# Kernel tuning notes

Hardware: AMD Instinct MI355X
Metric: run time of the kernel (lower is better)

Reference implementation:

```python
import jax, jax.numpy as jnp
import numpy as np

HEADS = 16
DIM_HEAD = 64
SCALE = DIM_HEAD ** -0.5
EPS = 1e-5


def layer_norm(x, gamma):
    mu = jnp.mean(x, axis=-1, keepdims=True)
    var = jnp.var(x, axis=-1, keepdims=True)
    return (x - mu) * jax.lax.rsqrt(var + EPS) * gamma


def setup_inputs() -> dict:
    key = jax.random.key(0)
    ks = jax.random.split(key, 5)
    B, S, D = 2, 2048, 1024
    x = jax.random.normal(ks[0], (B, S, D), dtype=jnp.float32)
    gamma = jnp.ones((D,), dtype=jnp.float32)
    Wq = jax.random.normal(ks[1], (D, HEADS * DIM_HEAD), dtype=jnp.float32) * (D ** -0.5)
    Wkv = jax.random.normal(ks[2], (D, 2 * DIM_HEAD), dtype=jnp.float32) * (D ** -0.5)
    Wo = jax.random.normal(ks[3], (HEADS * DIM_HEAD, D), dtype=jnp.float32) * ((HEADS * DIM_HEAD) ** -0.5)
    return {"x": x, "gamma": gamma, "Wq": Wq, "Wkv": Wkv, "Wo": Wo}


def reference(x, gamma, Wq, Wkv, Wo):
    B, S, D = x.shape
    kv_input = x  # context=None -> self attention
    xn = layer_norm(x, gamma)
    q = xn @ Wq                          # [B,S,H*Dh]
    kv = kv_input @ Wkv                  # [B,S,2*Dh]
    k, v = jnp.split(kv, 2, axis=-1)     # each [B,S,Dh]
    q = q.reshape(B, S, HEADS, DIM_HEAD).transpose(0, 2, 1, 3) * SCALE  # [B,H,S,Dh]
    sim = jnp.einsum('bhid,bjd->bhij', q, k)  # [B,H,S,S]
    # causal mask: triu(j - i + 1) masked
    i_idx = jnp.arange(S)[:, None]
    j_idx = jnp.arange(S)[None, :]
    neg = -jnp.finfo(sim.dtype).max
    sim = jnp.where(j_idx > i_idx, neg, sim)
    attn = jax.nn.softmax(sim, axis=-1)
    out = jnp.einsum('bhij,bjd->bhid', attn, v)  # [B,H,S,Dh]
    out = out.transpose(0, 2, 1, 3).reshape(B, S, HEADS * DIM_HEAD)
    return out @ Wo
```

## Files before the change

### kernel.cpp

```cpp
#include <hip/hip_runtime.h>

typedef unsigned short u16;
typedef __attribute__((ext_vector_type(8))) u16    u16x8;
typedef __attribute__((ext_vector_type(4))) u16    u16x4;
typedef __attribute__((ext_vector_type(2))) unsigned u32x2;
typedef __attribute__((ext_vector_type(8))) __bf16 bf16x8;
typedef __attribute__((ext_vector_type(4))) float  f32x4;
typedef __attribute__((ext_vector_type(16))) float f32x16;

__device__ __forceinline__ u16 f2bf(float f) {
    unsigned u = __float_as_uint(f);
    u += 0x7fffu + ((u >> 16) & 1u);
    return (u16)(u >> 16);
}
__device__ __forceinline__ bf16x8 ldbf8(const u16* p) {
    return __builtin_bit_cast(bf16x8, *(const u16x8*)p);
}
__device__ __forceinline__ f32x4 mfma16(bf16x8 a, bf16x8 b, f32x4 c) {
    return __builtin_amdgcn_mfma_f32_16x16x32_bf16(a, b, c, 0, 0, 0);
}
__device__ __forceinline__ f32x16 mfma32x(bf16x8 a, bf16x8 b, f32x16 c) {
    return __builtin_amdgcn_mfma_f32_32x32x16_bf16(a, b, c, 0, 0, 0);
}
__device__ __forceinline__ float exp2a(float x) {
    float r; asm("v_exp_f32 %0, %1" : "=v"(r) : "v"(x)); return r;
}
__device__ __forceinline__ unsigned cvtpk(float lo, float hiv) {
    unsigned r; asm("v_cvt_pk_bf16_f32 %0, %1, %2" : "=v"(r) : "v"(lo), "v"(hiv)); return r;
}
__device__ __forceinline__ u32x2 permswap2(unsigned a, unsigned b) {
    return __builtin_amdgcn_permlane32_swap(a, b, false, false);
}
__device__ __forceinline__ float combine_sum(float x) {
    u32x2 pr = permswap2(__float_as_uint(x), __float_as_uint(x));
    return __uint_as_float(pr[0]) + __uint_as_float(pr[1]);
}
__device__ __forceinline__ bf16x8 pack4(unsigned a, unsigned b, unsigned c, unsigned d) {
    union { unsigned u[4]; bf16x8 v; } t; t.u[0] = a; t.u[1] = b; t.u[2] = c; t.u[3] = d; return t.v;
}

__global__ void transpose_cast_all(const float* __restrict__ Wq, const float* __restrict__ Wkv,
                                   const float* __restrict__ Wo, u16* __restrict__ Wq_t,
                                   u16* __restrict__ Wkv_t, u16* __restrict__ Wo_t, float qscale) {
    __shared__ float tile[32][33];
    int by = blockIdx.y;
    const float* W; u16* Wt; int N; float scale;
    if (by < 32)      { W = Wq;  Wt = Wq_t;  N = 1024; scale = qscale; }
    else if (by < 36) { W = Wkv; Wt = Wkv_t; N = 128;  by -= 32; scale = 1.0f; }
    else              { W = Wo;  Wt = Wo_t;  N = 1024; by -= 36; scale = 1.0f; }
    const int K = 1024;
    int kb = blockIdx.x * 32, nb = by * 32;
    int tx = threadIdx.x, ty = threadIdx.y;
#pragma unroll
    for (int i = 0; i < 32; i += 8)
        tile[ty + i][tx] = W[(size_t)(kb + ty + i) * N + nb + tx];
    __syncthreads();
#pragma unroll
    for (int i = 0; i < 32; i += 8)
        Wt[(size_t)(nb + ty + i) * K + kb + tx] = f2bf(tile[tx][ty + i] * scale);
}

__global__ __launch_bounds__(256) void ln_cast(const float* __restrict__ x, const float* __restrict__ gamma,
                                               u16* __restrict__ xn, u16* __restrict__ xb) {
    const int row = blockIdx.x;
    const int t = threadIdx.x;
    const float4 v = ((const float4*)(x + (size_t)row * 1024))[t];
    float s  = v.x + v.y + v.z + v.w;
    float s2 = v.x * v.x + v.y * v.y + v.z * v.z + v.w * v.w;
#pragma unroll
    for (int off = 32; off; off >>= 1) { s += __shfl_down(s, off); s2 += __shfl_down(s2, off); }
    __shared__ float red[2][4];
    const int w = t >> 6, lane = t & 63;
    if (lane == 0) { red[0][w] = s; red[1][w] = s2; }
    __syncthreads();
    s  = red[0][0] + red[0][1] + red[0][2] + red[0][3];
    s2 = red[1][0] + red[1][1] + red[1][2] + red[1][3];
    const float mu  = s * (1.0f / 1024.0f);
    const float var = s2 * (1.0f / 1024.0f) - mu * mu;
    const float rs  = rsqrtf(var + 1e-5f);
    const float4 g = ((const float4*)gamma)[t];
    u16x4 on, ob;
    on.x = f2bf((v.x - mu) * rs * g.x); on.y = f2bf((v.y - mu) * rs * g.y);
    on.z = f2bf((v.z - mu) * rs * g.z); on.w = f2bf((v.w - mu) * rs * g.w);
    ob.x = f2bf(v.x); ob.y = f2bf(v.y); ob.z = f2bf(v.z); ob.w = f2bf(v.w);
    ((u16x4*)(xn + (size_t)row * 1024))[t] = on;
    ((u16x4*)(xb + (size_t)row * 1024))[t] = ob;
}

template<int BM, int BN, int BK, int EPI>
__global__ __launch_bounds__(256, 2) void gemm_bt(const u16* __restrict__ A, const u16* __restrict__ Bt,
                                                  u16* __restrict__ Cb, float* __restrict__ Cf,
                                                  u16* __restrict__ Cv, int M, int N, int K) {
    constexpr int WM = BM / 2, WN = BN / 2, FM = WM / 16, FN = WN / 16;
    constexpr int CPR = BK / 8;
    constexpr int MS = CPR - 1;
    constexpr int CHA = BM * CPR, CH = (BM + BN) * CPR, ITERS = CH / 256;
    __shared__ __align__(16) u16 lds[2][(BM + BN) * BK];
    __shared__ float kred[2][64];
    const int tid = threadIdx.x;
    const int nwg = gridDim.x * gridDim.y;
    int lin = blockIdx.x + gridDim.x * blockIdx.y;
    lin = (lin & 7) * (nwg >> 3) + (lin >> 3);
    const int bx = lin % gridDim.x, by = lin / gridDim.x;
    const int m0 = bx * BM, n0 = by * BN;
    const int w = tid >> 6, lane = tid & 63, cl = lane & 15, kg = lane >> 4;
    const int wr = w >> 1, wc = w & 1;

    auto stage = [&](int buf, int k0) {
#pragma unroll
        for (int it = 0; it < ITERS; ++it) {
            int c = it * 256 + tid;
            const u16* g;
            if (c < CHA) { int r = c / CPR, cc = c & MS; g = A  + (size_t)(m0 + r) * K + k0 + ((cc ^ (r & MS)) * 8); }
            else { int c2 = c - CHA; int r = c2 / CPR, cc = c2 & MS; g = Bt + (size_t)(n0 + r) * K + k0 + ((cc ^ (r & MS)) * 8); }
            __builtin_amdgcn_global_load_lds(
                (const __attribute__((address_space(1))) unsigned int*)g,
                (__attribute__((address_space(3))) unsigned int*)&lds[buf][c * 8], 16, 0, 0);
        }
    };

    const f32x4 zero = {0.f, 0.f, 0.f, 0.f};
    f32x4 acc[FM][FN];
#pragma unroll
    for (int m = 0; m < FM; m++)
#pragma unroll
        for (int n = 0; n < FN; n++) acc[m][n] = zero;

    const int KT = K / BK;
    stage(0, 0);
    for (int t = 0; t < KT; ++t) {
        __syncthreads();
        if (t + 1 < KT) stage((t + 1) & 1, (t + 1) * BK);
        const u16* As = &lds[t & 1][0];
        const u16* Bs = &lds[t & 1][BM * BK];
#pragma unroll
        for (int s = 0; s < BK / 32; s++) {
            bf16x8 af[FM], bfr[FN];
#pragma unroll
            for (int m = 0; m < FM; m++) {
                const int ra = wr * WM + m * 16 + cl;
                af[m] = ldbf8(As + ra * BK + (((s * 4 + kg) ^ (ra & MS)) * 8));
            }
#pragma unroll
            for (int n = 0; n < FN; n++) {
                const int rb = wc * WN + n * 16 + cl;
                bfr[n] = ldbf8(Bs + rb * BK + (((s * 4 + kg) ^ (rb & MS)) * 8));
            }
#pragma unroll
            for (int m = 0; m < FM; m++)
#pragma unroll
                for (int n = 0; n < FN; n++) acc[m][n] = mfma16(af[m], bfr[n], acc[m][n]);
        }
    }

#pragma unroll
    for (int m = 0; m < FM; m++)
#pragma unroll
        for (int n = 0; n < FN; n++)
#pragma unroll
            for (int r = 0; r < 4; r++) {
                const int row = m0 + wr * WM + m * 16 + kg * 4 + r;
                const int col = n0 + wc * WN + n * 16 + cl;
                const float v = acc[m][n][r];
                if constexpr (EPI == 0) Cb[(size_t)row * N + col] = f2bf(v);
                else if constexpr (EPI == 1) Cf[(size_t)row * N + col] = v;
                else {
                    if (col < 64) Cb[(size_t)row * 64 + col] = f2bf(v);
                    else { int bb = row >> 11, s = row & 2047;
                           Cv[((size_t)bb * 64 + (col - 64)) * 2048 + s] = f2bf(v); }
                }
            }

    if constexpr (EPI == 2) {
        if (n0 == 0) {
            float s2[FM][4];
#pragma unroll
            for (int m = 0; m < FM; m++)
#pragma unroll
                for (int r = 0; r < 4; r++) {
                    float t = 0.f;
#pragma unroll
                    for (int n = 0; n < FN; n++) {
                        const float vb = __uint_as_float(((unsigned)f2bf(acc[m][n][r])) << 16);
                        t = fmaf(vb, vb, t);
                    }
                    s2[m][r] = t;
                }
#pragma unroll
            for (int off = 1; off < 16; off <<= 1)
#pragma unroll
                for (int m = 0; m < FM; m++)
#pragma unroll
                    for (int r = 0; r < 4; r++) s2[m][r] += __shfl_xor(s2[m][r], off);
            if (cl == 0)
#pragma unroll
                for (int m = 0; m < FM; m++)
#pragma unroll
                    for (int r = 0; r < 4; r++) kred[wc][wr * 32 + m * 16 + kg * 4 + r] = s2[m][r];
            __syncthreads();
            if (tid < 64) {
                float t = kred[0][tid] + kred[1][tid];
#pragma unroll
                for (int off = 1; off < 64; off <<= 1) t = fmaxf(t, __shfl_xor(t, off));
                if (tid == 0) Cf[bx] = t;
            }
        }
    }
}

__global__ __launch_bounds__(256, 2) void attn_fwd(const u16* __restrict__ q, const u16* __restrict__ k,
                                                   const u16* __restrict__ vt, const float* __restrict__ kpart,
                                                   u16* __restrict__ o) {
    constexpr int S = 2048;
    const int bid = blockIdx.x;
    const int p = (bid < 256) ? (bid >> 5) : (15 - ((bid - 256) >> 5));
    const int bh = bid & 31;
    const int h = bh & 15, b = bh >> 4;
    const int tid = threadIdx.x, w = tid >> 6, lane = tid & 63;
    const int pw = w & 1, par = w >> 1;
    const int l31 = lane & 31;
    const bool hi = (lane & 32) != 0;
    const int hi1 = hi ? 1 : 0, hi8 = hi ? 8 : 0;
    const int t1 = 2 * p + pw, t2 = 63 - t1;
    const int iters = 32 - p;
    const size_t bS = (size_t)b * S;

    __shared__ __align__(16) u16 smem[18432];

    auto stageK = [&](int jt, int buf, int tl) {
        const int r = tid >> 3, c = tid & 7;
        const u16* gp = k + (bS + jt * 32 + r) * 64 + ((c ^ (r & 7)) * 8);
        __builtin_amdgcn_global_load_lds(
            (const __attribute__((address_space(1))) unsigned int*)gp,
            (__attribute__((address_space(3))) unsigned int*)(smem + (buf * 2 + tl) * 2048 + tid * 8), 16, 0, 0);
    };
    auto loadV = [&](int jt) -> u16x8 {
        const int rv = tid >> 2, c4 = tid & 3;
        return *(const u16x8*)(vt + ((size_t)b * 64 + rv) * S + jt * 32 + c4 * 8);
    };
    auto writeV = [&](int buf, int tl, u16x8 v) {
        const int rv = tid >> 2, c4 = tid & 3;
        *(u16x8*)(smem + 8192 + (buf * 2 + tl) * 2560 + rv * 40 + c4 * 8) = v;
    };

    float km = kpart[(b << 5) + l31];
#pragma unroll
    for (int off = 1; off < 32; off <<= 1) km = fmaxf(km, __shfl_xor(km, off));
    const float kmaxb = sqrtf(km);

    bf16x8 qf1[4], qf2[4];
    float mB1, mB2;
    auto qload = [&](int t, bf16x8 (&qf)[4]) -> float {
        const u16* qp = q + (bS + t * 32 + l31) * 1024 + h * 64 + hi8;
        float qn2 = 0.f;
#pragma unroll
        for (int sub = 0; sub < 4; sub++) {
            qf[sub] = ldbf8(qp + sub * 16);
            const u16x8 uv = __builtin_bit_cast(u16x8, qf[sub]);
#pragma unroll
            for (int j = 0; j < 8; j++) {
                const float v = __uint_as_float(((unsigned)uv[j]) << 16);
                qn2 = fmaf(v, v, qn2);
            }
        }
        return sqrtf(combine_sum(qn2)) * kmaxb;
    };
    mB1 = qload(t1, qf1);
    mB2 = qload(t2, qf2);

    f32x16 a1lo, a1hi, a2lo, a2hi;
#pragma unroll
    for (int r = 0; r < 16; r++) { a1lo[r] = 0.f; a1hi[r] = 0.f; a2lo[r] = 0.f; a2hi[r] = 0.f; }
    float l1 = 0.f, l2 = 0.f;

    auto process = [&](const bf16x8 (&qf)[4], const bf16x8 (&kf)[4],
                       const bf16x8& vf00, const bf16x8& vf01, const bf16x8& vf10, const bf16x8& vf11,
                       f32x16& a0, f32x16& a1, float& lr, float mB, bool diag) {
        f32x16 s;
#pragma unroll
        for (int r = 0; r < 16; r++) s[r] = 0.f;
#pragma unroll
        for (int sub = 0; sub < 4; sub++) s = mfma32x(kf[sub], qf[sub], s);
        if (diag) {
#pragma unroll
            for (int r = 0; r < 16; r++) {
                const int kvl = (r & 3) + 8 * (r >> 2) + (hi ? 4 : 0);
                if (kvl > l31) s[r] = -1e30f;
            }
        }
        float p0 = 0.f, p1 = 0.f;
#pragma unroll
        for (int r = 0; r < 16; r += 2) {
            const float ea = exp2a(s[r] - mB);
            const float eb = exp2a(s[r + 1] - mB);
            s[r] = ea; s[r + 1] = eb;
            p0 += ea; p1 += eb;
        }
        lr += p0 + p1;
        unsigned w0 = cvtpk(s[0], s[1]),  w1 = cvtpk(s[2], s[3]);
        unsigned w2 = cvtpk(s[4], s[5]),  w3 = cvtpk(s[6], s[7]);
        u32x2 r02 = permswap2(w0, w2), r13 = permswap2(w1, w3);
        bf16x8 pf0 = pack4(r02[0], r13[0], r02[1], r13[1]);
        unsigned y0 = cvtpk(s[8], s[9]),   y1 = cvtpk(s[10], s[11]);
        unsigned y2 = cvtpk(s[12], s[13]), y3 = cvtpk(s[14], s[15]);
        u32x2 t02 = permswap2(y0, y2), t13 = permswap2(y1, y3);
        bf16x8 pf1 = pack4(t02[0], t13[0], t02[1], t13[1]);
        a0 = mfma32x(vf00, pf0, a0);
        a0 = mfma32x(vf01, pf1, a0);
        a1 = mfma32x(vf10, pf0, a1);
        a1 = mfma32x(vf11, pf1, a1);
    };

    stageK(0, 0, 0); stageK(1, 0, 1);
    u16x8 v0 = loadV(0), v1 = loadV(1);
    for (int i = 0; i < iters; i++) {
        const int buf = i & 1;
        writeV(buf, 0, v0); writeV(buf, 1, v1);
        __syncthreads();
        if (i + 1 < iters) {
            stageK(2 * i + 2, buf ^ 1, 0); stageK(2 * i + 3, buf ^ 1, 1);
            v0 = loadV(2 * i + 2); v1 = loadV(2 * i + 3);
        }
        const int jt = 2 * i + par;
        if (jt <= t2) {
            const u16* kcur = smem + (buf * 2 + par) * 2048;
            const u16* vcur = smem + 8192 + (buf * 2 + par) * 2560;
            bf16x8 kf[4];
#pragma unroll
            for (int sub = 0; sub < 4; sub++)
                kf[sub] = ldbf8(kcur + l31 * 64 + (((sub * 2 + hi1) ^ (l31 & 7)) * 8));
            const bf16x8 vf00 = ldbf8(vcur + l31 * 40 + hi8);
            const bf16x8 vf01 = ldbf8(vcur + l31 * 40 + 16 + hi8);
            const bf16x8 vf10 = ldbf8(vcur + (32 + l31) * 40 + hi8);
            const bf16x8 vf11 = ldbf8(vcur + (32 + l31) * 40 + 16 + hi8);
            if (jt <= t1) process(qf1, kf, vf00, vf01, vf10, vf11, a1lo, a1hi, l1, mB1, jt == t1);
            process(qf2, kf, vf00, vf01, vf10, vf11, a2lo, a2hi, l2, mB2, jt == t2);
        }
    }
    float l1t = combine_sum(l1), l2t = combine_sum(l2);

    float* fm = (float*)smem;
    __syncthreads();
    {
        float* dst = fm + (((pw * 2) + (par ? 0 : 1)) * 64 + lane) * 36;
        if (par) { *(f32x16*)dst = a1lo; *(f32x16*)(dst + 16) = a1hi; dst[32] = l1t; }
        else     { *(f32x16*)dst = a2lo; *(f32x16*)(dst + 16) = a2hi; dst[32] = l2t; }
    }
    __syncthreads();
    {
        const float* src = fm + (((pw * 2) + (par ? 1 : 0)) * 64 + lane) * 36;
        const f32x16 s0 = *(const f32x16*)src;
        const f32x16 s1 = *(const f32x16*)(src + 16);
        if (par) {
#pragma unroll
            for (int r = 0; r < 16; r++) { a2lo[r] += s0[r]; a2hi[r] += s1[r]; }
            l2t += src[32];
        } else {
#pragma unroll
            for (int r = 0; r < 16; r++) { a1lo[r] += s0[r]; a1hi[r] += s1[r]; }
            l1t += src[32];
        }
    }
    __syncthreads();

    auto epi = [&](const f32x16& a0, const f32x16& a1, float lt, int t) {
        const float rl = 1.0f / lt;
        u16* lb = smem + w * 2304;
#pragma unroll
        for (int i = 0; i < 8; i++) {
            const int d = ((2 * i) & 3) + 8 * ((2 * i) >> 2) + (hi ? 4 : 0);
            *(unsigned*)&lb[l31 * 72 + d]      = cvtpk(a0[2 * i] * rl, a0[2 * i + 1] * rl);
            *(unsigned*)&lb[l31 * 72 + 32 + d] = cvtpk(a1[2 * i] * rl, a1[2 * i + 1] * rl);
        }
        asm volatile("s_waitcnt lgkmcnt(0)" ::: "memory");
#pragma unroll
        for (int i = 0; i < 4; i++) {
            const int qq = i * 8 + (lane >> 3), dd = (lane & 7) * 8;
            *(u16x8*)(o + (bS + t * 32 + qq) * 1024 + h * 64 + dd) = *(const u16x8*)&lb[qq * 72 + dd];
        }
    };
    if (par == 0) epi(a1lo, a1hi, l1t, t1);
    else          epi(a2lo, a2hi, l2t, t2);
}

extern "C" void kernel_launch(void* const* d_in, const int* in_sizes, int n_in,
                              void* d_out, int out_size, void* d_ws, size_t ws_size,
                              hipStream_t stream) {
    const float* x     = (const float*)d_in[0];
    const float* gamma = (const float*)d_in[1];
    const float* Wq    = (const float*)d_in[2];
    const float* Wkv   = (const float*)d_in[3];
    const float* Wo    = (const float*)d_in[4];
    float* out = (float*)d_out;
    char* ws = (char*)d_ws;

    u16* Wq_t  = (u16*)(ws + 0);
    u16* Wo_t  = (u16*)(ws + (2u << 20));
    u16* Wkv_t = (u16*)(ws + (4u << 20));
    u16* xn    = (u16*)(ws + 4456448u);
    u16* xb    = (u16*)(ws + 12845056u);
    u16* qb    = (u16*)(ws + 21233664u);
    u16* kb    = (u16*)(ws + 29622272u);
    u16* vtb   = (u16*)(ws + 30146560u);
    u16* attb  = (u16*)(ws + 30670848u);
    float* kpart = (float*)xb;

    const float qscale = 0.125f * 1.44269504f;
    transpose_cast_all<<<dim3(32, 68), dim3(32, 8), 0, stream>>>(Wq, Wkv, Wo, Wq_t, Wkv_t, Wo_t, qscale);

    ln_cast<<<4096, 256, 0, stream>>>(x, gamma, xn, xb);

    gemm_bt<128, 64, 64, 0><<<dim3(32, 16), 256, 0, stream>>>(xn, Wq_t, qb, nullptr, nullptr, 4096, 1024, 1024);
    gemm_bt<64, 64, 32, 2><<<dim3(64, 2), 256, 0, stream>>>(xb, Wkv_t, kb, kpart, vtb, 4096, 128, 1024);
    attn_fwd<<<512, 256, 0, stream>>>(qb, kb, vtb, kpart, attb);
    gemm_bt<128, 64, 64, 1><<<dim3(32, 16), 256, 0, stream>>>(attb, Wo_t, nullptr, out, nullptr, 4096, 1024, 1024);
}
```

Baseline: 94.45 us.

## Merge prep kernels and fuse Q and KV projections into one launch

Combines the layer-norm/cast kernel and the weight transpose kernel into a single launch, and merges the Q projection GEMM with the KV projection GEMM into one grid of 576 blocks sharing a 128x64 tile core. The KV GEMM now uses the larger tile, so the per-block key-norm partial max covers 128 rows, and the attention kernel reduces 16 partials instead of 32. The softmax offset is folded into the MFMA accumulator init, saving a subtract per element. This cuts launch count and the tail of the small KV GEMM, at the cost of a more complex block dispatch and a dedicated kpart buffer.

```diff
diff --git a/kernel.cpp b/kernel.cpp
--- a/kernel.cpp
+++ b/kernel.cpp
@@ -39,69 +39,66 @@
     union { unsigned u[4]; bf16x8 v; } t; t.u[0] = a; t.u[1] = b; t.u[2] = c; t.u[3] = d; return t.v;
 }
 
-__global__ void transpose_cast_all(const float* __restrict__ Wq, const float* __restrict__ Wkv,
-                                   const float* __restrict__ Wo, u16* __restrict__ Wq_t,
-                                   u16* __restrict__ Wkv_t, u16* __restrict__ Wo_t, float qscale) {
-    __shared__ float tile[32][33];
-    int by = blockIdx.y;
-    const float* W; u16* Wt; int N; float scale;
-    if (by < 32)      { W = Wq;  Wt = Wq_t;  N = 1024; scale = qscale; }
-    else if (by < 36) { W = Wkv; Wt = Wkv_t; N = 128;  by -= 32; scale = 1.0f; }
-    else              { W = Wo;  Wt = Wo_t;  N = 1024; by -= 36; scale = 1.0f; }
-    const int K = 1024;
-    int kb = blockIdx.x * 32, nb = by * 32;
-    int tx = threadIdx.x, ty = threadIdx.y;
-#pragma unroll
-    for (int i = 0; i < 32; i += 8)
-        tile[ty + i][tx] = W[(size_t)(kb + ty + i) * N + nb + tx];
-    __syncthreads();
-#pragma unroll
-    for (int i = 0; i < 32; i += 8)
-        Wt[(size_t)(nb + ty + i) * K + kb + tx] = f2bf(tile[tx][ty + i] * scale);
-}
-
-__global__ __launch_bounds__(256) void ln_cast(const float* __restrict__ x, const float* __restrict__ gamma,
-                                               u16* __restrict__ xn, u16* __restrict__ xb) {
-    const int row = blockIdx.x;
-    const int t = threadIdx.x;
-    const float4 v = ((const float4*)(x + (size_t)row * 1024))[t];
-    float s  = v.x + v.y + v.z + v.w;
-    float s2 = v.x * v.x + v.y * v.y + v.z * v.z + v.w * v.w;
-#pragma unroll
-    for (int off = 32; off; off >>= 1) { s += __shfl_down(s, off); s2 += __shfl_down(s2, off); }
-    __shared__ float red[2][4];
-    const int w = t >> 6, lane = t & 63;
-    if (lane == 0) { red[0][w] = s; red[1][w] = s2; }
-    __syncthreads();
-    s  = red[0][0] + red[0][1] + red[0][2] + red[0][3];
-    s2 = red[1][0] + red[1][1] + red[1][2] + red[1][3];
-    const float mu  = s * (1.0f / 1024.0f);
-    const float var = s2 * (1.0f / 1024.0f) - mu * mu;
-    const float rs  = rsqrtf(var + 1e-5f);
-    const float4 g = ((const float4*)gamma)[t];
-    u16x4 on, ob;
-    on.x = f2bf((v.x - mu) * rs * g.x); on.y = f2bf((v.y - mu) * rs * g.y);
-    on.z = f2bf((v.z - mu) * rs * g.z); on.w = f2bf((v.w - mu) * rs * g.w);
-    ob.x = f2bf(v.x); ob.y = f2bf(v.y); ob.z = f2bf(v.z); ob.w = f2bf(v.w);
-    ((u16x4*)(xn + (size_t)row * 1024))[t] = on;
-    ((u16x4*)(xb + (size_t)row * 1024))[t] = ob;
-}
-
-template<int BM, int BN, int BK, int EPI>
-__global__ __launch_bounds__(256, 2) void gemm_bt(const u16* __restrict__ A, const u16* __restrict__ Bt,
-                                                  u16* __restrict__ Cb, float* __restrict__ Cf,
-                                                  u16* __restrict__ Cv, int M, int N, int K) {
-    constexpr int WM = BM / 2, WN = BN / 2, FM = WM / 16, FN = WN / 16;
-    constexpr int CPR = BK / 8;
-    constexpr int MS = CPR - 1;
+__global__ __launch_bounds__(256) void prep_kernel(const float* __restrict__ x, const float* __restrict__ gamma,
+                                                   const float* __restrict__ Wq, const float* __restrict__ Wkv,
+                                                   const float* __restrict__ Wo, u16* __restrict__ xn,
+                                                   u16* __restrict__ xb, u16* __restrict__ Wq_t,
+                                                   u16* __restrict__ Wkv_t, u16* __restrict__ Wo_t, float qscale) {
+    const int bid = blockIdx.x, tid = threadIdx.x;
+    if (bid < 4096) {
+        const int row = bid;
+        const float4 v = ((const float4*)(x + (size_t)row * 1024))[tid];
+        float s  = v.x + v.y + v.z + v.w;
+        float s2 = v.x * v.x + v.y * v.y + v.z * v.z + v.w * v.w;
+#pragma unroll
+        for (int off = 32; off; off >>= 1) { s += __shfl_down(s, off); s2 += __shfl_down(s2, off); }
+        __shared__ float red[2][4];
+        const int w = tid >> 6, lane = tid & 63;
+        if (lane == 0) { red[0][w] = s; red[1][w] = s2; }
+        __syncthreads();
+        s  = red[0][0] + red[0][1] + red[0][2] + red[0][3];
+        s2 = red[1][0] + red[1][1] + red[1][2] + red[1][3];
+        const float mu  = s * (1.0f / 1024.0f);
+        const float var = s2 * (1.0f / 1024.0f) - mu * mu;
+        const float rs  = rsqrtf(var + 1e-5f);
+        const float4 g = ((const float4*)gamma)[tid];
+        u16x4 on, ob;
+        on.x = f2bf((v.x - mu) * rs * g.x); on.y = f2bf((v.y - mu) * rs * g.y);
+        on.z = f2bf((v.z - mu) * rs * g.z); on.w = f2bf((v.w - mu) * rs * g.w);
+        ob.x = f2bf(v.x); ob.y = f2bf(v.y); ob.z = f2bf(v.z); ob.w = f2bf(v.w);
+        ((u16x4*)(xn + (size_t)row * 1024))[tid] = on;
+        ((u16x4*)(xb + (size_t)row * 1024))[tid] = ob;
+    } else {
+        __shared__ float tile[32][33];
+        int bt = bid - 4096;
+        int by = bt >> 5;
+        const float* W; u16* Wt; int N; float scale;
+        if (by < 32)      { W = Wq;  Wt = Wq_t;  N = 1024; scale = qscale; }
+        else if (by < 36) { W = Wkv; Wt = Wkv_t; N = 128;  by -= 32; scale = 1.0f; }
+        else              { W = Wo;  Wt = Wo_t;  N = 1024; by -= 36; scale = 1.0f; }
+        const int K = 1024;
+        const int kb = (bt & 31) * 32, nb = by * 32;
+        const int tx = tid & 31, ty = tid >> 5;
+#pragma unroll
+        for (int i = 0; i < 32; i += 8)
+            tile[ty + i][tx] = W[(size_t)(kb + ty + i) * N + nb + tx];
+        __syncthreads();
+#pragma unroll
+        for (int i = 0; i < 32; i += 8)
+            Wt[(size_t)(nb + ty + i) * K + kb + tx] = f2bf(tile[tx][ty + i] * scale);
+    }
+}
+
+template<int EPI>
+__device__ __forceinline__ void gemm_core(u16* lds, float (*kred)[128],
+                                          const u16* __restrict__ A, const u16* __restrict__ Bt,
+                                          u16* __restrict__ Cb, float* __restrict__ Cf, u16* __restrict__ Cv,
+                                          int N, int K, int bx, int by, int tid) {
+    constexpr int BM = 128, BN = 64, BK = 64;
+    constexpr int WM = 64, WN = 32, FM = 4, FN = 2;
+    constexpr int CPR = BK / 8, MS = CPR - 1;
     constexpr int CHA = BM * CPR, CH = (BM + BN) * CPR, ITERS = CH / 256;
-    __shared__ __align__(16) u16 lds[2][(BM + BN) * BK];
-    __shared__ float kred[2][64];
-    const int tid = threadIdx.x;
-    const int nwg = gridDim.x * gridDim.y;
-    int lin = blockIdx.x + gridDim.x * blockIdx.y;
-    lin = (lin & 7) * (nwg >> 3) + (lin >> 3);
-    const int bx = lin % gridDim.x, by = lin / gridDim.x;
+    constexpr int LB = (BM + BN) * BK;
     const int m0 = bx * BM, n0 = by * BN;
     const int w = tid >> 6, lane = tid & 63, cl = lane & 15, kg = lane >> 4;
     const int wr = w >> 1, wc = w & 1;
@@ -115,7 +112,7 @@
             else { int c2 = c - CHA; int r = c2 / CPR, cc = c2 & MS; g = Bt + (size_t)(n0 + r) * K + k0 + ((cc ^ (r & MS)) * 8); }
             __builtin_amdgcn_global_load_lds(
                 (const __attribute__((address_space(1))) unsigned int*)g,
-                (__attribute__((address_space(3))) unsigned int*)&lds[buf][c * 8], 16, 0, 0);
+                (__attribute__((address_space(3))) unsigned int*)&lds[buf * LB + c * 8], 16, 0, 0);
         }
     };
 
@@ -131,8 +128,8 @@
     for (int t = 0; t < KT; ++t) {
         __syncthreads();
         if (t + 1 < KT) stage((t + 1) & 1, (t + 1) * BK);
-        const u16* As = &lds[t & 1][0];
-        const u16* Bs = &lds[t & 1][BM * BK];
+        const u16* As = &lds[(t & 1) * LB];
+        const u16* Bs = &lds[(t & 1) * LB + BM * BK];
 #pragma unroll
         for (int s = 0; s < BK / 32; s++) {
             bf16x8 af[FM], bfr[FN];
@@ -196,16 +193,41 @@
 #pragma unroll
                 for (int m = 0; m < FM; m++)
 #pragma unroll
-                    for (int r = 0; r < 4; r++) kred[wc][wr * 32 + m * 16 + kg * 4 + r] = s2[m][r];
+                    for (int r = 0; r < 4; r++) kred[wc][wr * 64 + m * 16 + kg * 4 + r] = s2[m][r];
             __syncthreads();
             if (tid < 64) {
-                float t = kred[0][tid] + kred[1][tid];
+                float t = fmaxf(kred[0][tid] + kred[1][tid], kred[0][tid + 64] + kred[1][tid + 64]);
 #pragma unroll
                 for (int off = 1; off < 64; off <<= 1) t = fmaxf(t, __shfl_xor(t, off));
                 if (tid == 0) Cf[bx] = t;
             }
         }
     }
+}
+
+__global__ __launch_bounds__(256, 2) void gemm_qkv(const u16* __restrict__ xn, const u16* __restrict__ Wq_t,
+                                                   u16* __restrict__ qb, const u16* __restrict__ xb,
+                                                   const u16* __restrict__ Wkv_t, u16* __restrict__ kb,
+                                                   u16* __restrict__ vtb, float* __restrict__ kpart) {
+    __shared__ __align__(16) u16 lds[2 * 192 * 64];
+    __shared__ float kred[2][128];
+    const int tid = threadIdx.x;
+    const int nwg = gridDim.x;
+    int lin = blockIdx.x;
+    lin = (lin & 7) * (nwg >> 3) + (lin >> 3);
+    if (lin < 512) gemm_core<0>(lds, kred, xn, Wq_t, qb, nullptr, nullptr, 1024, 1024, lin & 31, lin >> 5, tid);
+    else { int l2 = lin - 512; gemm_core<2>(lds, kred, xb, Wkv_t, kb, kpart, vtb, 128, 1024, l2 & 31, l2 >> 5, tid); }
+}
+
+__global__ __launch_bounds__(256, 2) void gemm_o(const u16* __restrict__ attb, const u16* __restrict__ Wo_t,
+                                                 float* __restrict__ out) {
+    __shared__ __align__(16) u16 lds[2 * 192 * 64];
+    __shared__ float kred[2][128];
+    const int tid = threadIdx.x;
+    const int nwg = gridDim.x;
+    int lin = blockIdx.x;
+    lin = (lin & 7) * (nwg >> 3) + (lin >> 3);
+    gemm_core<1>(lds, kred, attb, Wo_t, nullptr, out, nullptr, 1024, 1024, lin & 31, lin >> 5, tid);
 }
 
 __global__ __launch_bounds__(256, 2) void attn_fwd(const u16* __restrict__ q, const u16* __restrict__ k,
@@ -243,9 +265,9 @@
         *(u16x8*)(smem + 8192 + (buf * 2 + tl) * 2560 + rv * 40 + c4 * 8) = v;
     };
 
-    float km = kpart[(b << 5) + l31];
-#pragma unroll
-    for (int off = 1; off < 32; off <<= 1) km = fmaxf(km, __shfl_xor(km, off));
+    float km = kpart[(b << 4) + (l31 & 15)];
+#pragma unroll
+    for (int off = 1; off < 16; off <<= 1) km = fmaxf(km, __shfl_xor(km, off));
     const float kmaxb = sqrtf(km);
 
     bf16x8 qf1[4], qf2[4];
@@ -278,7 +300,7 @@
                        f32x16& a0, f32x16& a1, float& lr, float mB, bool diag) {
         f32x16 s;
 #pragma unroll
-        for (int r = 0; r < 16; r++) s[r] = 0.f;
+        for (int r = 0; r < 16; r++) s[r] = -mB;
 #pragma unroll
         for (int sub = 0; sub < 4; sub++) s = mfma32x(kf[sub], qf[sub], s);
         if (diag) {
@@ -291,8 +313,8 @@
         float p0 = 0.f, p1 = 0.f;
 #pragma unroll
         for (int r = 0; r < 16; r += 2) {
-            const float ea = exp2a(s[r] - mB);
-            const float eb = exp2a(s[r + 1] - mB);
+            const float ea = exp2a(s[r]);
+            const float eb = exp2a(s[r + 1]);
             s[r] = ea; s[r + 1] = eb;
             p0 += ea; p1 += eb;
         }
@@ -403,15 +425,11 @@
     u16* kb    = (u16*)(ws + 29622272u);
     u16* vtb   = (u16*)(ws + 30146560u);
     u16* attb  = (u16*)(ws + 30670848u);
-    float* kpart = (float*)xb;
+    float* kpart = (float*)(ws + 39059456u);
 
     const float qscale = 0.125f * 1.44269504f;
-    transpose_cast_all<<<dim3(32, 68), dim3(32, 8), 0, stream>>>(Wq, Wkv, Wo, Wq_t, Wkv_t, Wo_t, qscale);
-
-    ln_cast<<<4096, 256, 0, stream>>>(x, gamma, xn, xb);
-
-    gemm_bt<128, 64, 64, 0><<<dim3(32, 16), 256, 0, stream>>>(xn, Wq_t, qb, nullptr, nullptr, 4096, 1024, 1024);
-    gemm_bt<64, 64, 32, 2><<<dim3(64, 2), 256, 0, stream>>>(xb, Wkv_t, kb, kpart, vtb, 4096, 128, 1024);
+    prep_kernel<<<4096 + 2176, 256, 0, stream>>>(x, gamma, Wq, Wkv, Wo, xn, xb, Wq_t, Wkv_t, Wo_t, qscale);
+    gemm_qkv<<<576, 256, 0, stream>>>(xn, Wq_t, qb, xb, Wkv_t, kb, vtb, kpart);
     attn_fwd<<<512, 256, 0, stream>>>(qb, kb, vtb, kpart, attb);
-    gemm_bt<128, 64, 64, 1><<<dim3(32, 16), 256, 0, stream>>>(attb, Wo_t, nullptr, out, nullptr, 4096, 1024, 1024);
-}
+    gemm_o<<<512, 256, 0, stream>>>(attb, Wo_t, out);
+}
```

New measurement: 79.47 us (median of 2 runs). 1.19x faster.
